# Kernel tuning notes

Measured on AMD Instinct MI355X. Metric: run time of the kernel, lower is better.

## Reference

```python
import jax, jax.numpy as jnp
import numpy as np

K = 3  # kernel_size
PAD = K // 2


def setup_inputs() -> dict:
    key = jax.random.key(0)
    k1, k2 = jax.random.split(key)
    B, C, H, W = 8, 64, 128, 128
    x = jax.random.normal(k1, (B, C, H, W), dtype=jnp.float32)
    dynamic_kernel = jax.random.normal(k2, (B, C, K * K, H, W), dtype=jnp.float32)
    return {"x": x, "dynamic_kernel": dynamic_kernel}


def reference(x, dynamic_kernel):
    # x: [B,C,H,W]; dynamic_kernel: [B,C,K^2,H,W]
    B, C, H, W = x.shape
    xp = jnp.pad(x, ((0, 0), (0, 0), (PAD, PAD), (PAD, PAD)))
    # F.unfold patch ordering: (ki, kj) row-major, matching view(B,C,K*K,H,W)
    patches = jnp.stack(
        [xp[:, :, i:i + H, j:j + W] for i in range(K) for j in range(K)],
        axis=2,
    )  # [B,C,K^2,H,W]
    out = (patches * dynamic_kernel).sum(axis=2)  # [B,C,H,W]
    return out
```

## Files before the change

### kernel.cpp

```cpp
#include <hip/hip_runtime.h>


constexpr int Bc = 8, Cc = 64, Hc = 128, Wc = 128;
constexpr int HW = Hc * Wc;

typedef float f32x4 __attribute__((ext_vector_type(4)));

__global__ __launch_bounds__(256) void adaconv2d_kernel(
    const float* __restrict__ x,
    const float* __restrict__ dk,
    float* __restrict__ out)
{
    int tid  = blockIdx.x * blockDim.x + threadIdx.x;
    int w0   = (tid & 31) << 2;
    int rest = tid >> 5;
    int h    = rest & (Hc - 1);
    int bc   = (Bc * Cc - 1) - (rest >> 7);

    const float* xp = x + bc * HW;
    const float* kp = dk + (long long)bc * 9 * HW + h * Wc + w0;

    float xr[3][6];
    #pragma unroll
    for (int r = 0; r < 3; ++r) {
        int hh = h + r - 1;
        if (hh >= 0 && hh < Hc) {
            const float* row = xp + hh * Wc;
            f32x4 m = *reinterpret_cast<const f32x4*>(row + w0);
            xr[r][1] = m.x; xr[r][2] = m.y; xr[r][3] = m.z; xr[r][4] = m.w;
            xr[r][0] = (w0 > 0)      ? row[w0 - 1] : 0.f;
            xr[r][5] = (w0 + 4 < Wc) ? row[w0 + 4] : 0.f;
        } else {
            #pragma unroll
            for (int j = 0; j < 6; ++j) xr[r][j] = 0.f;
        }
    }

    float acc[4];
    #pragma unroll
    for (int j = 0; j < 4; ++j) acc[j] = 0.f;

    #pragma unroll
    for (int r = 0; r < 3; ++r) {
        #pragma unroll
        for (int s = 0; s < 3; ++s) {
            f32x4 k = *reinterpret_cast<const f32x4*>(kp + (r * 3 + s) * HW);
            acc[0] += xr[r][s + 0] * k.x;
            acc[1] += xr[r][s + 1] * k.y;
            acc[2] += xr[r][s + 2] * k.z;
            acc[3] += xr[r][s + 3] * k.w;
        }
    }

    f32x4 o = { acc[0], acc[1], acc[2], acc[3] };
    __builtin_nontemporal_store(o, reinterpret_cast<f32x4*>(out + bc * HW + h * Wc + w0));
}

extern "C" void kernel_launch(void* const* d_in, const int* in_sizes, int n_in,
                              void* d_out, int out_size, void* d_ws, size_t ws_size,
                              hipStream_t stream) {
    const float* x  = (const float*)d_in[0];
    const float* dk = (const float*)d_in[1];
    float* out      = (float*)d_out;

    const int total_quads = Bc * Cc * Hc * (Wc / 4);
    const int block = 256;
    const int grid  = total_quads / block;
    adaconv2d_kernel<<<grid, block, 0, stream>>>(x, dk, out);
}
```

Before: 418.4 us.

## Use persistent grid with register double-buffered prefetch of dynamic kernel weights

Launches a fixed grid of 2048 blocks in which each thread handles four (b,c) planes in a loop, instead of one quad per thread. The nine dynamic-kernel vector loads for the next iteration are issued into a second register buffer before the current iteration's FMAs, so memory latency overlaps with compute. This aims to keep more loads in flight on a purely bandwidth-bound kernel, at the cost of higher register use (18 float4 buffers) and possibly lower occupancy. The reversed bc ordering of the old version is dropped.

After: 417.1 us. Within noise of the previous version (-0.3%).

```diff
diff --git a/kernel.cpp b/kernel.cpp
--- a/kernel.cpp
+++ b/kernel.cpp
@@ -3,24 +3,17 @@
 
 constexpr int Bc = 8, Cc = 64, Hc = 128, Wc = 128;
 constexpr int HW = Hc * Wc;
+constexpr int TPB = 256;
+constexpr int NBLK = 2048;
+constexpr int NTHR = NBLK * TPB;
+constexpr int QUADS = Bc * Cc * Hc * (Wc / 4);
+constexpr int ITERS = QUADS / NTHR;
+constexpr int BCSTEP = NTHR >> 12;
 
 typedef float f32x4 __attribute__((ext_vector_type(4)));
 
-__global__ __launch_bounds__(256) void adaconv2d_kernel(
-    const float* __restrict__ x,
-    const float* __restrict__ dk,
-    float* __restrict__ out)
-{
-    int tid  = blockIdx.x * blockDim.x + threadIdx.x;
-    int w0   = (tid & 31) << 2;
-    int rest = tid >> 5;
-    int h    = rest & (Hc - 1);
-    int bc   = (Bc * Cc - 1) - (rest >> 7);
-
-    const float* xp = x + bc * HW;
-    const float* kp = dk + (long long)bc * 9 * HW + h * Wc + w0;
-
-    float xr[3][6];
+__device__ __forceinline__ void load_x6(const float* __restrict__ xp,
+                                        int h, int w0, float xr[3][6]) {
     #pragma unroll
     for (int r = 0; r < 3; ++r) {
         int hh = h + r - 1;
@@ -35,25 +28,60 @@
             for (int j = 0; j < 6; ++j) xr[r][j] = 0.f;
         }
     }
+}
 
-    float acc[4];
-    #pragma unroll
-    for (int j = 0; j < 4; ++j) acc[j] = 0.f;
+__global__ __launch_bounds__(256) void adaconv2d_kernel(
+    const float* __restrict__ x,
+    const float* __restrict__ dk,
+    float* __restrict__ out)
+{
+    int tid = blockIdx.x * TPB + threadIdx.x;
+    int w0  = (tid & 31) << 2;
+    int h   = (tid >> 5) & (Hc - 1);
+    int bc0 = tid >> 12;
+
+    const float* kbase = dk + (long long)bc0 * 9 * HW + h * Wc + w0;
+    const long long KSTEP = (long long)BCSTEP * 9 * HW;
+
+    f32x4 kv[2][9];
 
     #pragma unroll
-    for (int r = 0; r < 3; ++r) {
+    for (int t = 0; t < 9; ++t)
+        kv[0][t] = *reinterpret_cast<const f32x4*>(kbase + t * HW);
+
+    #pragma unroll
+    for (int i = 0; i < ITERS; ++i) {
+        const int cur = i & 1;
+        const int nxt = cur ^ 1;
+        const int bc  = bc0 + i * BCSTEP;
+
+        float xr[3][6];
+        load_x6(x + bc * HW, h, w0, xr);
+
+        if (i + 1 < ITERS) {
+            const float* kn = kbase + (long long)(i + 1) * KSTEP;
+            #pragma unroll
+            for (int t = 0; t < 9; ++t)
+                kv[nxt][t] = *reinterpret_cast<const f32x4*>(kn + t * HW);
+        }
+
+        float acc[4] = {0.f, 0.f, 0.f, 0.f};
         #pragma unroll
-        for (int s = 0; s < 3; ++s) {
-            f32x4 k = *reinterpret_cast<const f32x4*>(kp + (r * 3 + s) * HW);
-            acc[0] += xr[r][s + 0] * k.x;
-            acc[1] += xr[r][s + 1] * k.y;
-            acc[2] += xr[r][s + 2] * k.z;
-            acc[3] += xr[r][s + 3] * k.w;
+        for (int r = 0; r < 3; ++r) {
+            #pragma unroll
+            for (int s = 0; s < 3; ++s) {
+                f32x4 k = kv[cur][r * 3 + s];
+                acc[0] += xr[r][s + 0] * k.x;
+                acc[1] += xr[r][s + 1] * k.y;
+                acc[2] += xr[r][s + 2] * k.z;
+                acc[3] += xr[r][s + 3] * k.w;
+            }
         }
+
+        f32x4 o = { acc[0], acc[1], acc[2], acc[3] };
+        __builtin_nontemporal_store(
+            o, reinterpret_cast<f32x4*>(out + bc * HW + h * Wc + w0));
     }
-
-    f32x4 o = { acc[0], acc[1], acc[2], acc[3] };
-    __builtin_nontemporal_store(o, reinterpret_cast<f32x4*>(out + bc * HW + h * Wc + w0));
 }
 
 extern "C" void kernel_launch(void* const* d_in, const int* in_sizes, int n_in,
@@ -63,8 +91,5 @@
     const float* dk = (const float*)d_in[1];
     float* out      = (float*)d_out;
 
-    const int total_quads = Bc * Cc * Hc * (Wc / 4);
-    const int block = 256;
-    const int grid  = total_quads / block;
-    adaconv2d_kernel<<<grid, block, 0, stream>>>(x, dk, out);
+    adaconv2d_kernel<<<NBLK, TPB, 0, stream>>>(x, dk, out);
 }
```
